# Optimization experiments

Hardware: AMD Instinct MI355X
Metric: run time of the kernel (lower is better)

Reference implementation:

```python
import jax, jax.numpy as jnp
import numpy as np

B, S, HID = 1, 2048, 2048
NH, NKV = 16, 4
HD = HID // NH  # 128


def _rope_manual(x, cos_h, sin_h):
    # x: [B, S, nh, HD]; cos_h/sin_h: [1, S, 1, HD//2]
    d = x.shape[-1]
    x_rot = x[..., : d // 2]
    x_pass = x[..., d // 2:]
    # rotate interleaved pairs inside the first half
    x_rot = jnp.stack([-x_rot[..., 1::2], x_rot[..., ::2]], axis=-1)
    x_rot = x_rot.reshape(x_rot.shape[:-2] + (d // 2,))
    return jnp.concatenate(
        [x_rot * cos_h + x_pass * sin_h, -x_rot * sin_h + x_pass * cos_h], axis=-1
    )


def setup_inputs() -> dict:
    key = jax.random.key(0)
    ks = jax.random.split(key, 7)
    bound = 1.0 / np.sqrt(HID)
    return {
        "x": jax.random.normal(ks[0], (B, S, HID), jnp.float32),
        "cos": jax.random.uniform(ks[1], (S, HD), jnp.float32),
        "sin": jax.random.uniform(ks[2], (S, HD), jnp.float32),
        "wq": jax.random.uniform(ks[3], (NH * HD, HID), jnp.float32, -bound, bound),
        "wk": jax.random.uniform(ks[4], (NKV * HD, HID), jnp.float32, -bound, bound),
        "wv": jax.random.uniform(ks[5], (NKV * HD, HID), jnp.float32, -bound, bound),
        "wo": jax.random.uniform(ks[6], (HID, HID), jnp.float32, -bound, bound),
    }


def reference(x, cos, sin, wq, wk, wv, wo):
    b, s, _ = x.shape
    q = jnp.einsum("bsh,oh->bso", x, wq).reshape(b, s, NH, HD)
    k = jnp.einsum("bsh,oh->bso", x, wk).reshape(b, s, NKV, HD)
    v = jnp.einsum("bsh,oh->bso", x, wv).reshape(b, s, NKV, HD)

    cos_h = cos[None, :, None, : HD // 2]  # [1,S,1,HD/2]
    sin_h = sin[None, :, None, : HD // 2]
    q = _rope_manual(q, cos_h, sin_h)
    k = _rope_manual(k, cos_h, sin_h)

    # [B, H, S, D]
    q = q.transpose(0, 2, 1, 3)
    k = k.transpose(0, 2, 1, 3)
    v = v.transpose(0, 2, 1, 3)
    # GQA kv repeat (repeat_interleave over head dim)
    rep = NH // NKV
    k = jnp.repeat(k, rep, axis=1)
    v = jnp.repeat(v, rep, axis=1)

    scale = 1.0 / np.sqrt(HD).astype(np.float32)
    scores = jnp.einsum("bhqd,bhkd->bhqk", q, k) * scale
    causal = jnp.tril(jnp.ones((s, s), bool))
    scores = jnp.where(causal[None, None], scores, jnp.finfo(scores.dtype).min)
    attn = jax.nn.softmax(scores, axis=-1)
    out = jnp.einsum("bhqk,bhkd->bhqd", attn, v)  # [B,H,S,D]
    out = out.transpose(0, 2, 1, 3).reshape(b, s, NH * HD)
    return jnp.einsum("bso,ho->bsh", out, wo)
```

## Files before the change

kernel.cpp:

```cpp
#include <hip/hip_runtime.h>
#include <hip/hip_bf16.h>

typedef __bf16 bf16_t;
typedef __attribute__((ext_vector_type(8))) __bf16 bf16x8;
typedef __attribute__((ext_vector_type(4))) __bf16 bf16x4;
typedef __attribute__((ext_vector_type(4))) float f32x4;

#define S_LEN 2048
#define HID 2048
#define NH 16
#define NKV 4
#define HD 128

__device__ __forceinline__ void gll16(const bf16_t* g, bf16_t* l) {
    __builtin_amdgcn_global_load_lds(
        (const __attribute__((address_space(1))) unsigned int*)g,
        (__attribute__((address_space(3))) unsigned int*)l, 16, 0, 0);
}

__device__ __forceinline__ bf16x8 cvt2x4(float4 a, float4 b) {
    bf16x8 o;
    o[0]=(bf16_t)a.x; o[1]=(bf16_t)a.y; o[2]=(bf16_t)a.z; o[3]=(bf16_t)a.w;
    o[4]=(bf16_t)b.x; o[5]=(bf16_t)b.y; o[6]=(bf16_t)b.z; o[7]=(bf16_t)b.w;
    return o;
}

__global__ __launch_bounds__(256) void cvt_f32_bf16(const float* __restrict__ in,
                                                    bf16_t* __restrict__ out, int n)
{
    int i = (blockIdx.x * 256 + threadIdx.x) * 8;
    if (i >= n) return;
    float4 a = *(const float4*)&in[i];
    float4 b = *(const float4*)&in[i + 4];
    *(bf16x8*)&out[i] = cvt2x4(a, b);
}

__global__ __launch_bounds__(256) void cvt_w3(const float* __restrict__ wq,
                                              const float* __restrict__ wk,
                                              const float* __restrict__ wv,
                                              bf16_t* __restrict__ out)
{
    int i = (blockIdx.x * 256 + threadIdx.x) * 8;
    const float* src; int off;
    if (i < 4 * 1024 * 1024)      { src = wq; off = i; }
    else if (i < 5 * 1024 * 1024) { src = wk; off = i - 4 * 1024 * 1024; }
    else                          { src = wv; off = i - 5 * 1024 * 1024; }
    float4 a = *(const float4*)&src[off];
    float4 b = *(const float4*)&src[off + 4];
    *(bf16x8*)&out[i] = cvt2x4(a, b);
}

template<int MODE, typename CT>
__global__ __launch_bounds__(256, 4) void gemm128x64(
    const bf16_t* __restrict__ A, const bf16_t* __restrict__ B,
    CT* __restrict__ C, bf16_t* __restrict__ CkP, bf16_t* __restrict__ CvtP,
    int N, int K)
{
    __shared__ __align__(16) bf16_t sA[128 * 64];
    __shared__ __align__(16) bf16_t sB[64 * 64];

    const int tid = threadIdx.x, lane = tid & 63, wave = tid >> 6;
    const int l16 = lane & 15, quad = lane >> 4;
    const int m0 = blockIdx.y * 128, n0 = blockIdx.x * 64;
    const int wm = (wave >> 1) * 64, wn = (wave & 1) * 32;

    const bf16_t* gA[4]; const bf16_t* gB[2];
    bf16_t* lA[4]; bf16_t* lB[2];
#pragma unroll
    for (int t = 0; t < 4; t++) {
        int p = (wave * 4 + t) * 64 + lane;
        int row = p >> 3;
        int lc = (p & 7) ^ (row & 7);
        gA[t] = A + (size_t)(m0 + row) * K + lc * 8;
        lA[t] = &sA[(wave * 4 + t) * 512];
    }
#pragma unroll
    for (int t = 0; t < 2; t++) {
        int p = (wave * 2 + t) * 64 + lane;
        int row = p >> 3;
        int lc = (p & 7) ^ (row & 7);
        gB[t] = B + (size_t)(n0 + row) * K + lc * 8;
        lB[t] = &sB[(wave * 2 + t) * 512];
    }

    int offA[2][4], offB[2][2];
#pragma unroll
    for (int kc = 0; kc < 2; kc++) {
#pragma unroll
        for (int i = 0; i < 4; i++) {
            int rm = wm + i * 16 + l16;
            offA[kc][i] = rm * 64 + (((kc * 4 + quad) ^ (rm & 7)) * 8);
        }
#pragma unroll
        for (int j = 0; j < 2; j++) {
            int rn = wn + j * 16 + l16;
            offB[kc][j] = rn * 64 + (((kc * 4 + quad) ^ (rn & 7)) * 8);
        }
    }

    f32x4 acc[4][2] = {};

    for (int k0 = 0; k0 < K; k0 += 64) {
        __syncthreads();
#pragma unroll
        for (int t = 0; t < 4; t++) { gll16(gA[t], lA[t]); gA[t] += 64; }
#pragma unroll
        for (int t = 0; t < 2; t++) { gll16(gB[t], lB[t]); gB[t] += 64; }
        __syncthreads();

#pragma unroll
        for (int kc = 0; kc < 2; kc++) {
            bf16x8 af[4], bfv[2];
#pragma unroll
            for (int i = 0; i < 4; i++) af[i] = *(bf16x8*)&sA[offA[kc][i]];
#pragma unroll
            for (int j = 0; j < 2; j++) bfv[j] = *(bf16x8*)&sB[offB[kc][j]];
#pragma unroll
            for (int i = 0; i < 4; i++)
#pragma unroll
                for (int j = 0; j < 2; j++)
                    acc[i][j] = __builtin_amdgcn_mfma_f32_16x16x32_bf16(af[i], bfv[j], acc[i][j], 0, 0, 0);
        }
    }

#pragma unroll
    for (int i = 0; i < 4; i++) {
        int rowb = m0 + wm + i * 16 + quad * 4;
#pragma unroll
        for (int j = 0; j < 2; j++) {
            int col = n0 + wn + j * 16 + l16;
#pragma unroll
            for (int r = 0; r < 4; r++) {
                float v = acc[i][j][r];
                int row = rowb + r;
                if (MODE == 0) {
                    C[(size_t)row * N + col] = (CT)v;
                } else {
                    if (col < 2048)      C[(size_t)row * 2048 + col] = (CT)v;
                    else if (col < 2560) CkP[(size_t)row * 512 + (col - 2048)] = (bf16_t)v;
                    else                 CvtP[(size_t)(col - 2560) * S_LEN + row] = (bf16_t)v;
                }
            }
        }
    }
}

__global__ void rope_all(bf16_t* __restrict__ Qh, bf16_t* __restrict__ Kh,
                         const float* __restrict__ cosb, const float* __restrict__ sinb)
{
    int s = blockIdx.x;
    int grp = blockIdx.y;
    int sub = threadIdx.x >> 5;
    int i = threadIdx.x & 31;
    bf16_t* row = (grp < 4) ? (Qh + ((size_t)s * NH + grp * 4 + sub) * HD)
                            : (Kh + ((size_t)s * NKV + sub) * HD);
    float x0 = (float)row[2 * i];
    float x1 = (float)row[2 * i + 1];
    float p0 = (float)row[64 + 2 * i];
    float p1 = (float)row[64 + 2 * i + 1];
    float c0 = cosb[s * HD + 2 * i];
    float c1 = cosb[s * HD + 2 * i + 1];
    float n0 = sinb[s * HD + 2 * i];
    float n1 = sinb[s * HD + 2 * i + 1];
    float r0 = -x1, r1 = x0;
    row[2 * i]          = (bf16_t)(r0 * c0 + p0 * n0);
    row[2 * i + 1]      = (bf16_t)(r1 * c1 + p1 * n1);
    row[64 + 2 * i]     = (bf16_t)(-r0 * n0 + p0 * c0);
    row[64 + 2 * i + 1] = (bf16_t)(-r1 * n1 + p1 * c1);
}

__global__ __launch_bounds__(512, 2) void flash_attn9(
    const bf16_t* __restrict__ Q,
    const bf16_t* __restrict__ Kb,
    const bf16_t* __restrict__ VT,
    bf16_t* __restrict__ OpD,
    bf16_t* __restrict__ OpX,
    float* __restrict__ lpart,
    int S)
{
    __shared__ __align__(16) bf16_t sK[64 * 136];
    __shared__ __align__(16) bf16_t sVT[2][128 * 72];
    __shared__ __align__(16) bf16_t sP[8][16 * 72];

    const int c   = blockIdx.x;
    const int kvh = blockIdx.y;
    int qt = 0, cb = 0;
    while (cb + 1 + (qt >> 3) <= c) { cb += 1 + (qt >> 3); qt++; }
    const int ci     = c - cb;
    const int splits = 1 + (qt >> 3);
    const int ntiles = qt + 1;
    const int tb = (ci * ntiles) / splits;
    const int te = ((ci + 1) * ntiles) / splits;

    const int q0  = qt * 64;
    const int tid = threadIdx.x, lane = tid & 63, wave = tid >> 6;
    const int l16 = lane & 15, quad = lane >> 4;
    const int rowg = wave & 3;
    const int h0   = kvh * 4 + (wave >> 2) * 2;
    const float scale = 0.08838834764831845f;

    const int qrow = q0 + rowg * 16 + l16;

    bf16x8 qf[2][4];
#pragma unroll
    for (int h = 0; h < 2; h++)
#pragma unroll
        for (int cc = 0; cc < 4; cc++)
            qf[h][cc] = *(const bf16x8*)&Q[(size_t)qrow * HID + (h0 + h) * HD + cc * 32 + quad * 8];

    f32x4 oacc[2][8] = {};
    float lsum[2] = {0.f, 0.f};

    int krow[2], kcol[2], vrow[2], vcol[2];
#pragma unroll
    for (int it = 0; it < 2; it++) {
        int cc = tid + 512 * it;
        krow[it] = cc >> 4; kcol[it] = (cc & 15) * 8;
        vrow[it] = cc >> 3; vcol[it] = (cc & 7) * 8;
    }

    bf16x8 kpre[2], vpre[2];
#pragma unroll
    for (int it = 0; it < 2; it++) {
        kpre[it] = *(const bf16x8*)&Kb[(size_t)(tb * 64 + krow[it]) * (NKV * HD) + kvh * HD + kcol[it]];
        vpre[it] = *(const bf16x8*)&VT[((size_t)kvh * HD + vrow[it]) * S + tb * 64 + vcol[it]];
    }
#pragma unroll
    for (int it = 0; it < 2; it++) {
        *(bf16x8*)&sK[krow[it] * 136 + kcol[it]] = kpre[it];
        *(bf16x8*)&sVT[0][vrow[it] * 72 + vcol[it]] = vpre[it];
    }
    if (tb + 1 < te) {
        const int t1 = (tb + 1) * 64;
#pragma unroll
        for (int it = 0; it < 2; it++) {
            kpre[it] = *(const bf16x8*)&Kb[(size_t)(t1 + krow[it]) * (NKV * HD) + kvh * HD + kcol[it]];
            vpre[it] = *(const bf16x8*)&VT[((size_t)kvh * HD + vrow[it]) * S + t1 + vcol[it]];
        }
    }
    __syncthreads();

    int sel = 0;
    for (int kt = tb; kt < te; kt++) {
        const int t0 = kt * 64;
        const int ns = sel ^ 1;

        f32x4 sc[2][4];
        __builtin_amdgcn_s_setprio(1);
#pragma unroll
        for (int nt = 0; nt < 4; nt++) {
            bf16x8 kf[4];
#pragma unroll
            for (int cc = 0; cc < 4; cc++)
                kf[cc] = *(bf16x8*)&sK[(nt * 16 + l16) * 136 + cc * 32 + quad * 8];
#pragma unroll
            for (int h = 0; h < 2; h++) {
                f32x4 d = {};
#pragma unroll
                for (int cc = 0; cc < 4; cc++)
                    d = __builtin_amdgcn_mfma_f32_16x16x32_bf16(kf[cc], qf[h][cc], d, 0, 0, 0);
                sc[h][nt] = d;
            }
        }
        __builtin_amdgcn_s_setprio(0);

        __syncthreads();

        if (kt + 1 < te) {
#pragma unroll
            for (int it = 0; it < 2; it++) {
                *(bf16x8*)&sK[krow[it] * 136 + kcol[it]] = kpre[it];
                *(bf16x8*)&sVT[ns][vrow[it] * 72 + vcol[it]] = vpre[it];
            }
            if (kt + 2 < te) {
                const int t2 = t0 + 128;
#pragma unroll
                for (int it = 0; it < 2; it++) {
                    kpre[it] = *(const bf16x8*)&Kb[(size_t)(t2 + krow[it]) * (NKV * HD) + kvh * HD + kcol[it]];
                    vpre[it] = *(const bf16x8*)&VT[((size_t)kvh * HD + vrow[it]) * S + t2 + vcol[it]];
                }
            }
        }

        bf16x8 pa[2][2];
        if (kt == qt) {
#pragma unroll
            for (int h = 0; h < 2; h++) {
#pragma unroll
                for (int nt = 0; nt < 4; nt++) {
                    const int tbk = t0 + nt * 16 + quad * 4;
                    bf16x4 pk;
#pragma unroll
                    for (int r = 0; r < 4; r++) {
                        float p = (tbk + r <= qrow) ? __expf(sc[h][nt][r] * scale) : 0.0f;
                        lsum[h] += p;
                        pk[r] = (bf16_t)p;
                    }
                    *(bf16x4*)&sP[wave][l16 * 72 + nt * 16 + quad * 4] = pk;
                }
#pragma unroll
                for (int kc = 0; kc < 2; kc++)
                    pa[h][kc] = *(bf16x8*)&sP[wave][l16 * 72 + kc * 32 + quad * 8];
            }
        } else {
#pragma unroll
            for (int h = 0; h < 2; h++) {
#pragma unroll
                for (int nt = 0; nt < 4; nt++) {
                    bf16x4 pk;
#pragma unroll
                    for (int r = 0; r < 4; r++) {
                        float p = __expf(sc[h][nt][r] * scale);
                        lsum[h] += p;
                        pk[r] = (bf16_t)p;
                    }
                    *(bf16x4*)&sP[wave][l16 * 72 + nt * 16 + quad * 4] = pk;
                }
#pragma unroll
                for (int kc = 0; kc < 2; kc++)
                    pa[h][kc] = *(bf16x8*)&sP[wave][l16 * 72 + kc * 32 + quad * 8];
            }
        }

        __builtin_amdgcn_s_setprio(1);
#pragma unroll
        for (int dt = 0; dt < 8; dt++)
#pragma unroll
            for (int kc = 0; kc < 2; kc++) {
                bf16x8 vf = *(bf16x8*)&sVT[sel][(dt * 16 + l16) * 72 + kc * 32 + quad * 8];
#pragma unroll
                for (int h = 0; h < 2; h++)
                    oacc[h][dt] = __builtin_amdgcn_mfma_f32_16x16x32_bf16(pa[h][kc], vf, oacc[h][dt], 0, 0, 0);
            }
        __builtin_amdgcn_s_setprio(0);

        __syncthreads();
        sel = ns;
    }

    const int sg = kvh * 80 + c;
    bf16_t* Op = (sg < 256) ? (OpD + (size_t)sg * 32768)
                            : (OpX + (size_t)(sg - 256) * 32768);
#pragma unroll
    for (int h = 0; h < 2; h++) {
        const int hl = (wave >> 2) * 2 + h;
        float lr = lsum[h];
        lr += __shfl_xor(lr, 16, 64);
        lr += __shfl_xor(lr, 32, 64);
        if (quad == 0)
            lpart[(size_t)sg * 256 + (rowg * 16 + l16) * 4 + hl] = lr;
#pragma unroll
        for (int r = 0; r < 4; r++) {
            int rr = rowg * 16 + quad * 4 + r;
#pragma unroll
            for (int dt = 0; dt < 8; dt++)
                Op[((size_t)rr * 4 + hl) * 128 + dt * 16 + l16] =
                    (bf16_t)(oacc[h][dt][r]);
        }
    }
}

__global__ __launch_bounds__(256) void flash_combine9(
    const bf16_t* __restrict__ OpD, const bf16_t* __restrict__ OpX,
    const float* __restrict__ lpart, bf16_t* __restrict__ oh)
{
    int i = (blockIdx.x * 256 + threadIdx.x) * 8;
    int s = i >> 11;
    int h = (i >> 7) & 15;
    int col = i & 127;
    int qt = s >> 6;
    int f = qt >> 3;
    int base = qt + 4 * f * (f - 1) + (qt & 7) * f;
    int splits = 1 + f;
    int s0 = (h >> 2) * 80 + base;
    int roff = (s & 63) * 4 + (h & 3);
    float acc[8] = {0.f, 0.f, 0.f, 0.f, 0.f, 0.f, 0.f, 0.f};
    float l = 0.f;
    for (int ci = 0; ci < splits; ci++) {
        int sg = s0 + ci;
        const bf16_t* P = (sg < 256) ? (OpD + (size_t)sg * 32768)
                                     : (OpX + (size_t)(sg - 256) * 32768);
        bf16x8 a = *(const bf16x8*)&P[(size_t)roff * 128 + col];
#pragma unroll
        for (int j = 0; j < 8; j++) acc[j] += (float)a[j];
        l += lpart[(size_t)sg * 256 + roff];
    }
    float inv = 1.0f / l;
    bf16x8 o;
#pragma unroll
    for (int j = 0; j < 8; j++)
        o[j] = (bf16_t)(acc[j] * inv);
    *(bf16x8*)&oh[i] = o;
}

extern "C" void kernel_launch(void* const* d_in, const int* in_sizes, int n_in,
                              void* d_out, int out_size, void* d_ws, size_t ws_size,
                              hipStream_t stream)
{
    const float* x    = (const float*)d_in[0];
    const float* cosb = (const float*)d_in[1];
    const float* sinb = (const float*)d_in[2];
    const float* wq   = (const float*)d_in[3];
    const float* wk   = (const float*)d_in[4];
    const float* wv   = (const float*)d_in[5];
    const float* wo   = (const float*)d_in[6];
    float* out = (float*)d_out;

    char* ws = (char*)d_ws;
    bf16_t* wb = (bf16_t*)(ws);
    bf16_t* qh = (bf16_t*)(ws + (size_t)12 * 1024 * 1024);
    bf16_t* kh = (bf16_t*)(ws + (size_t)20 * 1024 * 1024);
    bf16_t* vT = (bf16_t*)(ws + (size_t)22 * 1024 * 1024);
    float*  lp = (float*) (ws + (size_t)24 * 1024 * 1024);
    bf16_t* opx = (bf16_t*)(ws + (size_t)24 * 1024 * 1024 + 512 * 1024);
    bf16_t* xb  = (bf16_t*)d_out;
    bf16_t* opd = (bf16_t*)d_out;

    const int NX = S_LEN * HID;

    cvt_f32_bf16<<<NX / (256 * 8), 256, 0, stream>>>(x, xb, NX);

    cvt_w3<<<6 * 1024 * 1024 / (256 * 8), 256, 0, stream>>>(wq, wk, wv, wb);

    gemm128x64<1, bf16_t><<<dim3(48, 16), 256, 0, stream>>>(xb, wb, qh, kh, vT, 3072, HID);

    rope_all<<<dim3(S_LEN, 5), 128, 0, stream>>>(qh, kh, cosb, sinb);

    flash_attn9<<<dim3(80, NKV), 512, 0, stream>>>(qh, kh, vT, opd, opx, lp, S_LEN);

    flash_combine9<<<NX / (256 * 8), 256, 0, stream>>>(opd, opx, lp, qh);

    cvt_f32_bf16<<<NX / (256 * 8), 256, 0, stream>>>(wo, wb, NX);

    gemm128x64<0, float><<<dim3(32, 16), 256, 0, stream>>>(qh, wb, out, nullptr, nullptr, HID, HID);
}
```

Baseline: 228.0 us.

## Pair causal query tiles for balanced split-K work and double-buffer K in attention

```diff
diff --git a/kernel.cpp b/kernel.cpp
--- a/kernel.cpp
+++ b/kernel.cpp
@@ -169,7 +169,7 @@
     row[64 + 2 * i + 1] = (bf16_t)(-r1 * n1 + p1 * c1);
 }
 
-__global__ __launch_bounds__(512, 2) void flash_attn9(
+__global__ __launch_bounds__(512, 1) void flash_attn10(
     const bf16_t* __restrict__ Q,
     const bf16_t* __restrict__ Kb,
     const bf16_t* __restrict__ VT,
@@ -178,39 +178,23 @@
     float* __restrict__ lpart,
     int S)
 {
-    __shared__ __align__(16) bf16_t sK[64 * 136];
+    __shared__ __align__(16) bf16_t sK[2][64 * 136];
     __shared__ __align__(16) bf16_t sVT[2][128 * 72];
     __shared__ __align__(16) bf16_t sP[8][16 * 72];
 
     const int c   = blockIdx.x;
     const int kvh = blockIdx.y;
-    int qt = 0, cb = 0;
-    while (cb + 1 + (qt >> 3) <= c) { cb += 1 + (qt >> 3); qt++; }
-    const int ci     = c - cb;
-    const int splits = 1 + (qt >> 3);
-    const int ntiles = qt + 1;
-    const int tb = (ci * ntiles) / splits;
-    const int te = ((ci + 1) * ntiles) / splits;
-
-    const int q0  = qt * 64;
+    const int p   = c >> 2, sub = c & 3;
+    const int ts   = (33 * sub + 3) >> 2;
+    const int tend = (33 * sub + 36) >> 2;
+    const int tA   = p + 1;
+
     const int tid = threadIdx.x, lane = tid & 63, wave = tid >> 6;
     const int l16 = lane & 15, quad = lane >> 4;
     const int rowg = wave & 3;
     const int h0   = kvh * 4 + (wave >> 2) * 2;
     const float scale = 0.08838834764831845f;
 
-    const int qrow = q0 + rowg * 16 + l16;
-
-    bf16x8 qf[2][4];
-#pragma unroll
-    for (int h = 0; h < 2; h++)
-#pragma unroll
-        for (int cc = 0; cc < 4; cc++)
-            qf[h][cc] = *(const bf16x8*)&Q[(size_t)qrow * HID + (h0 + h) * HD + cc * 32 + quad * 8];
-
-    f32x4 oacc[2][8] = {};
-    float lsum[2] = {0.f, 0.f};
-
     int krow[2], kcol[2], vrow[2], vcol[2];
 #pragma unroll
     for (int it = 0; it < 2; it++) {
@@ -219,148 +203,173 @@
         vrow[it] = cc >> 3; vcol[it] = (cc & 7) * 8;
     }
 
-    bf16x8 kpre[2], vpre[2];
-#pragma unroll
-    for (int it = 0; it < 2; it++) {
-        kpre[it] = *(const bf16x8*)&Kb[(size_t)(tb * 64 + krow[it]) * (NKV * HD) + kvh * HD + kcol[it]];
-        vpre[it] = *(const bf16x8*)&VT[((size_t)kvh * HD + vrow[it]) * S + tb * 64 + vcol[it]];
-    }
-#pragma unroll
-    for (int it = 0; it < 2; it++) {
-        *(bf16x8*)&sK[krow[it] * 136 + kcol[it]] = kpre[it];
-        *(bf16x8*)&sVT[0][vrow[it] * 72 + vcol[it]] = vpre[it];
-    }
-    if (tb + 1 < te) {
-        const int t1 = (tb + 1) * 64;
+#pragma unroll
+    for (int sI = 0; sI < 2; sI++) {
+        int st0, st1, sqt, ssl;
+        if (sI == 0) {
+            if (ts < tA) { st0 = ts; st1 = (tend < tA ? tend : tA); sqt = p;      ssl = c; }
+            else         { st0 = ts; st1 = tend;                    sqt = 31 - p; ssl = c; }
+        } else {
+            if (!(ts < tA && tend > tA)) break;
+            st0 = tA; st1 = tend; sqt = 31 - p; ssl = 64 + p;
+        }
+        const int base = (sqt == p) ? 0 : tA;
+        const int kb = st0 - base, ke = st1 - base;
+        const int qt = sqt;
+        const int q0 = qt * 64;
+        const int qrow = q0 + rowg * 16 + l16;
+
+        bf16x8 qf[2][4];
+#pragma unroll
+        for (int h = 0; h < 2; h++)
+#pragma unroll
+            for (int cc = 0; cc < 4; cc++)
+                qf[h][cc] = *(const bf16x8*)&Q[(size_t)qrow * HID + (h0 + h) * HD + cc * 32 + quad * 8];
+
+        f32x4 oacc[2][8] = {};
+        float lsum[2] = {0.f, 0.f};
+
+        bf16x8 kpre[2], vpre[2];
 #pragma unroll
         for (int it = 0; it < 2; it++) {
-            kpre[it] = *(const bf16x8*)&Kb[(size_t)(t1 + krow[it]) * (NKV * HD) + kvh * HD + kcol[it]];
-            vpre[it] = *(const bf16x8*)&VT[((size_t)kvh * HD + vrow[it]) * S + t1 + vcol[it]];
-        }
-    }
-    __syncthreads();
-
-    int sel = 0;
-    for (int kt = tb; kt < te; kt++) {
-        const int t0 = kt * 64;
-        const int ns = sel ^ 1;
-
-        f32x4 sc[2][4];
-        __builtin_amdgcn_s_setprio(1);
-#pragma unroll
-        for (int nt = 0; nt < 4; nt++) {
-            bf16x8 kf[4];
-#pragma unroll
-            for (int cc = 0; cc < 4; cc++)
-                kf[cc] = *(bf16x8*)&sK[(nt * 16 + l16) * 136 + cc * 32 + quad * 8];
-#pragma unroll
-            for (int h = 0; h < 2; h++) {
-                f32x4 d = {};
+            kpre[it] = *(const bf16x8*)&Kb[(size_t)(kb * 64 + krow[it]) * (NKV * HD) + kvh * HD + kcol[it]];
+            vpre[it] = *(const bf16x8*)&VT[((size_t)kvh * HD + vrow[it]) * S + kb * 64 + vcol[it]];
+        }
+#pragma unroll
+        for (int it = 0; it < 2; it++) {
+            *(bf16x8*)&sK[0][krow[it] * 136 + kcol[it]] = kpre[it];
+            *(bf16x8*)&sVT[0][vrow[it] * 72 + vcol[it]] = vpre[it];
+        }
+        if (kb + 1 < ke) {
+            const int t1 = (kb + 1) * 64;
+#pragma unroll
+            for (int it = 0; it < 2; it++) {
+                kpre[it] = *(const bf16x8*)&Kb[(size_t)(t1 + krow[it]) * (NKV * HD) + kvh * HD + kcol[it]];
+                vpre[it] = *(const bf16x8*)&VT[((size_t)kvh * HD + vrow[it]) * S + t1 + vcol[it]];
+            }
+        }
+        __syncthreads();
+
+        int sel = 0;
+        for (int kt = kb; kt < ke; kt++) {
+            const int t0 = kt * 64;
+            const int ns = sel ^ 1;
+
+            if (kt + 1 < ke) {
+#pragma unroll
+                for (int it = 0; it < 2; it++) {
+                    *(bf16x8*)&sK[ns][krow[it] * 136 + kcol[it]] = kpre[it];
+                    *(bf16x8*)&sVT[ns][vrow[it] * 72 + vcol[it]] = vpre[it];
+                }
+                if (kt + 2 < ke) {
+                    const int t2 = t0 + 128;
+#pragma unroll
+                    for (int it = 0; it < 2; it++) {
+                        kpre[it] = *(const bf16x8*)&Kb[(size_t)(t2 + krow[it]) * (NKV * HD) + kvh * HD + kcol[it]];
+                        vpre[it] = *(const bf16x8*)&VT[((size_t)kvh * HD + vrow[it]) * S + t2 + vcol[it]];
+                    }
+                }
+            }
+
+            f32x4 sc[2][4];
+            __builtin_amdgcn_s_setprio(1);
+#pragma unroll
+            for (int nt = 0; nt < 4; nt++) {
+                bf16x8 kf[4];
 #pragma unroll
                 for (int cc = 0; cc < 4; cc++)
-                    d = __builtin_amdgcn_mfma_f32_16x16x32_bf16(kf[cc], qf[h][cc], d, 0, 0, 0);
-                sc[h][nt] = d;
-            }
-        }
-        __builtin_amdgcn_s_setprio(0);
-
-        __syncthreads();
-
-        if (kt + 1 < te) {
-#pragma unroll
-            for (int it = 0; it < 2; it++) {
-                *(bf16x8*)&sK[krow[it] * 136 + kcol[it]] = kpre[it];
-                *(bf16x8*)&sVT[ns][vrow[it] * 72 + vcol[it]] = vpre[it];
-            }
-            if (kt + 2 < te) {
-                const int t2 = t0 + 128;
-#pragma unroll
-                for (int it = 0; it < 2; it++) {
-                    kpre[it] = *(const bf16x8*)&Kb[(size_t)(t2 + krow[it]) * (NKV * HD) + kvh * HD + kcol[it]];
-                    vpre[it] = *(const bf16x8*)&VT[((size_t)kvh * HD + vrow[it]) * S + t2 + vcol[it]];
-                }
-            }
-        }
-
-        bf16x8 pa[2][2];
-        if (kt == qt) {
-#pragma unroll
-            for (int h = 0; h < 2; h++) {
-#pragma unroll
-                for (int nt = 0; nt < 4; nt++) {
-                    const int tbk = t0 + nt * 16 + quad * 4;
-                    bf16x4 pk;
-#pragma unroll
-                    for (int r = 0; r < 4; r++) {
-                        float p = (tbk + r <= qrow) ? __expf(sc[h][nt][r] * scale) : 0.0f;
-                        lsum[h] += p;
-                        pk[r] = (bf16_t)p;
+                    kf[cc] = *(bf16x8*)&sK[sel][(nt * 16 + l16) * 136 + cc * 32 + quad * 8];
+#pragma unroll
+                for (int h = 0; h < 2; h++) {
+                    f32x4 d = {};
+#pragma unroll
+                    for (int cc = 0; cc < 4; cc++)
+                        d = __builtin_amdgcn_mfma_f32_16x16x32_bf16(kf[cc], qf[h][cc], d, 0, 0, 0);
+                    sc[h][nt] = d;
+                }
+            }
+            __builtin_amdgcn_s_setprio(0);
+
+            bf16x8 pa[2][2];
+            if (kt == qt) {
+#pragma unroll
+                for (int h = 0; h < 2; h++) {
+#pragma unroll
+                    for (int nt = 0; nt < 4; nt++) {
+                        const int tbk = t0 + nt * 16 + quad * 4;
+                        bf16x4 pk;
+#pragma unroll
+                        for (int r = 0; r < 4; r++) {
+                            float pv = (tbk + r <= qrow) ? __expf(sc[h][nt][r] * scale) : 0.0f;
+                            lsum[h] += pv;
+                            pk[r] = (bf16_t)pv;
+                        }
+                        *(bf16x4*)&sP[wave][l16 * 72 + nt * 16 + quad * 4] = pk;
                     }
-                    *(bf16x4*)&sP[wave][l16 * 72 + nt * 16 + quad * 4] = pk;
-                }
-#pragma unroll
-                for (int kc = 0; kc < 2; kc++)
-                    pa[h][kc] = *(bf16x8*)&sP[wave][l16 * 72 + kc * 32 + quad * 8];
-            }
-        } else {
-#pragma unroll
-            for (int h = 0; h < 2; h++) {
-#pragma unroll
-                for (int nt = 0; nt < 4; nt++) {
-                    bf16x4 pk;
-#pragma unroll
-                    for (int r = 0; r < 4; r++) {
-                        float p = __expf(sc[h][nt][r] * scale);
-                        lsum[h] += p;
-                        pk[r] = (bf16_t)p;
+#pragma unroll
+                    for (int kc = 0; kc < 2; kc++)
+                        pa[h][kc] = *(bf16x8*)&sP[wave][l16 * 72 + kc * 32 + quad * 8];
+                }
+            } else {
+#pragma unroll
+                for (int h = 0; h < 2; h++) {
+#pragma unroll
+                    for (int nt = 0; nt < 4; nt++) {
+                        bf16x4 pk;
+#pragma unroll
+                        for (int r = 0; r < 4; r++) {
+                            float pv = __expf(sc[h][nt][r] * scale);
+                            lsum[h] += pv;
+                            pk[r] = (bf16_t)pv;
+                        }
+                        *(bf16x4*)&sP[wave][l16 * 72 + nt * 16 + quad * 4] = pk;
                     }
-                    *(bf16x4*)&sP[wave][l16 * 72 + nt * 16 + quad * 4] = pk;
-                }
-#pragma unroll
-                for (int kc = 0; kc < 2; kc++)
-                    pa[h][kc] = *(bf16x8*)&sP[wave][l16 * 72 + kc * 32 + quad * 8];
-            }
-        }
-
-        __builtin_amdgcn_s_setprio(1);
-#pragma unroll
-        for (int dt = 0; dt < 8; dt++)
-#pragma unroll
-            for (int kc = 0; kc < 2; kc++) {
-                bf16x8 vf = *(bf16x8*)&sVT[sel][(dt * 16 + l16) * 72 + kc * 32 + quad * 8];
-#pragma unroll
-                for (int h = 0; h < 2; h++)
-                    oacc[h][dt] = __builtin_amdgcn_mfma_f32_16x16x32_bf16(pa[h][kc], vf, oacc[h][dt], 0, 0, 0);
-            }
-        __builtin_amdgcn_s_setprio(0);
-
-        __syncthreads();
-        sel = ns;
-    }
-
-    const int sg = kvh * 80 + c;
-    bf16_t* Op = (sg < 256) ? (OpD + (size_t)sg * 32768)
-                            : (OpX + (size_t)(sg - 256) * 32768);
-#pragma unroll
-    for (int h = 0; h < 2; h++) {
-        const int hl = (wave >> 2) * 2 + h;
-        float lr = lsum[h];
-        lr += __shfl_xor(lr, 16, 64);
-        lr += __shfl_xor(lr, 32, 64);
-        if (quad == 0)
-            lpart[(size_t)sg * 256 + (rowg * 16 + l16) * 4 + hl] = lr;
-#pragma unroll
-        for (int r = 0; r < 4; r++) {
-            int rr = rowg * 16 + quad * 4 + r;
+#pragma unroll
+                    for (int kc = 0; kc < 2; kc++)
+                        pa[h][kc] = *(bf16x8*)&sP[wave][l16 * 72 + kc * 32 + quad * 8];
+                }
+            }
+
+            __builtin_amdgcn_s_setprio(1);
 #pragma unroll
             for (int dt = 0; dt < 8; dt++)
-                Op[((size_t)rr * 4 + hl) * 128 + dt * 16 + l16] =
-                    (bf16_t)(oacc[h][dt][r]);
-        }
-    }
-}
-
-__global__ __launch_bounds__(256) void flash_combine9(
+#pragma unroll
+                for (int kc = 0; kc < 2; kc++) {
+                    bf16x8 vf = *(bf16x8*)&sVT[sel][(dt * 16 + l16) * 72 + kc * 32 + quad * 8];
+#pragma unroll
+                    for (int h = 0; h < 2; h++)
+                        oacc[h][dt] = __builtin_amdgcn_mfma_f32_16x16x32_bf16(pa[h][kc], vf, oacc[h][dt], 0, 0, 0);
+                }
+            __builtin_amdgcn_s_setprio(0);
+
+            __syncthreads();
+            sel = ns;
+        }
+
+        const int sg = kvh * 80 + ssl;
+        bf16_t* Op = (sg < 256) ? (OpD + (size_t)sg * 32768)
+                                : (OpX + (size_t)(sg - 256) * 32768);
+#pragma unroll
+        for (int h = 0; h < 2; h++) {
+            const int hl = (wave >> 2) * 2 + h;
+            float lr = lsum[h];
+            lr += __shfl_xor(lr, 16, 64);
+            lr += __shfl_xor(lr, 32, 64);
+            if (quad == 0)
+                lpart[(size_t)sg * 256 + (rowg * 16 + l16) * 4 + hl] = lr;
+#pragma unroll
+            for (int r = 0; r < 4; r++) {
+                int rr = rowg * 16 + quad * 4 + r;
+#pragma unroll
+                for (int dt = 0; dt < 8; dt++)
+                    Op[((size_t)rr * 4 + hl) * 128 + dt * 16 + l16] =
+                        (bf16_t)(oacc[h][dt][r]);
+            }
+        }
+    }
+}
+
+__global__ __launch_bounds__(256) void flash_combine10(
     const bf16_t* __restrict__ OpD, const bf16_t* __restrict__ OpX,
     const float* __restrict__ lpart, bf16_t* __restrict__ oh)
 {
@@ -369,15 +378,31 @@
     int h = (i >> 7) & 15;
     int col = i & 127;
     int qt = s >> 6;
-    int f = qt >> 3;
-    int base = qt + 4 * f * (f - 1) + (qt & 7) * f;
-    int splits = 1 + f;
-    int s0 = (h >> 2) * 80 + base;
+    int base80 = (h >> 2) * 80;
     int roff = (s & 63) * 4 + (h & 3);
+
+    int sl[4]; int nsl = 0;
+    if (qt <= 15) {
+        int pr = qt;
+#pragma unroll
+        for (int sub = 0; sub < 4; sub++) {
+            int tss = (33 * sub + 3) >> 2;
+            if (tss < qt + 1) sl[nsl++] = pr * 4 + sub;
+        }
+    } else {
+        int pr = 31 - qt, tAh = pr + 1;
+#pragma unroll
+        for (int sub = 0; sub < 4; sub++) {
+            int tss = (33 * sub + 3) >> 2;
+            int ten = (33 * sub + 36) >> 2;
+            if (ten > tAh) sl[nsl++] = (tss < tAh) ? 64 + pr : pr * 4 + sub;
+        }
+    }
+
     float acc[8] = {0.f, 0.f, 0.f, 0.f, 0.f, 0.f, 0.f, 0.f};
     float l = 0.f;
-    for (int ci = 0; ci < splits; ci++) {
-        int sg = s0 + ci;
+    for (int ci = 0; ci < nsl; ci++) {
+        int sg = base80 + sl[ci];
         const bf16_t* P = (sg < 256) ? (OpD + (size_t)sg * 32768)
                                      : (OpX + (size_t)(sg - 256) * 32768);
         bf16x8 a = *(const bf16x8*)&P[(size_t)roff * 128 + col];
@@ -426,9 +451,9 @@
 
     rope_all<<<dim3(S_LEN, 5), 128, 0, stream>>>(qh, kh, cosb, sinb);
 
-    flash_attn9<<<dim3(80, NKV), 512, 0, stream>>>(qh, kh, vT, opd, opx, lp, S_LEN);
-
-    flash_combine9<<<NX / (256 * 8), 256, 0, stream>>>(opd, opx, lp, qh);
+    flash_attn10<<<dim3(64, NKV), 512, 0, stream>>>(qh, kh, vT, opd, opx, lp, S_LEN);
+
+    flash_combine10<<<NX / (256 * 8), 256, 0, stream>>>(opd, opx, lp, qh);
 
     cvt_f32_bf16<<<NX / (256 * 8), 256, 0, stream>>>(wo, wb, NX);
 
```

New measurement: 214.6 us. 1.06x faster.
